# Kernel optimization log

Hardware: AMD Instinct MI355X
Metric: run time of the kernel (lower is better)

Reference implementation:

```python
import jax, jax.numpy as jnp
import numpy as np

B, L, N, D = 4, 288, 170, 128
HEADS = 8
WS = 12        # window_size
SHIFT = 6      # shift_size
HID = 4 * D    # mlp hidden
NW = L // WS   # num windows
HD = D // HEADS
SCALE = HD ** -0.5
EPS = 1e-5


def _layernorm(x, g, b):
    m = jnp.mean(x, axis=-1, keepdims=True)
    v = jnp.mean(jnp.square(x - m), axis=-1, keepdims=True)
    return (x - m) * jax.lax.rsqrt(v + EPS) * g + b


def _attn_mask():
    # labels: [0:SHIFT]->0, [SHIFT:WS]->1, [WS:]->2 along L, then windowed
    idx = jnp.arange(L)
    lab = jnp.where(idx < SHIFT, 0.0, jnp.where(idx < WS, 1.0, 2.0)).astype(jnp.float32)
    mw = lab.reshape(NW, WS)                      # (nW, ws)
    diff = mw[:, None, :] - mw[:, :, None]        # (nW, ws, ws)
    return jnp.where(diff != 0, -100.0, 0.0)


def setup_inputs() -> dict:
    key = jax.random.key(0)
    ks = jax.random.split(key, 8)
    w = 0.02
    return {
        "x": jax.random.normal(ks[0], (B, L, N, D), jnp.float32),
        "qkv_w": jax.random.normal(ks[1], (D, 3 * D), jnp.float32) * w,
        "qkv_b": jnp.zeros((3 * D,), jnp.float32),
        "proj_w": jax.random.normal(ks[2], (D, D), jnp.float32) * w,
        "proj_b": jnp.zeros((D,), jnp.float32),
        "fc1_w": jax.random.normal(ks[3], (D, HID), jnp.float32) * w,
        "fc1_b": jnp.zeros((HID,), jnp.float32),
        "fc2_w": jax.random.normal(ks[4], (HID, D), jnp.float32) * w,
        "fc2_b": jnp.zeros((D,), jnp.float32),
        "g1": jnp.ones((D,), jnp.float32),
        "b1": jnp.zeros((D,), jnp.float32),
        "g2": jnp.ones((D,), jnp.float32),
        "b2": jnp.zeros((D,), jnp.float32),
    }


def reference(x, qkv_w, qkv_b, proj_w, proj_b, fc1_w, fc1_b, fc2_w, fc2_b, g1, b1, g2, b2):
    mask = _attn_mask()                                  # (nW, ws, ws)
    x = jnp.transpose(x, (0, 2, 1, 3))                   # (B, N, L, D)
    residual = x
    # shift + window partition
    sx = jnp.roll(x, SHIFT, axis=2)
    xw = sx.reshape(B, N, NW, WS, D).transpose(0, 2, 1, 3, 4).reshape(B * NW, N, WS, D)
    # windowed MSA
    qkv = xw @ qkv_w + qkv_b                             # (B_, N, ws, 3D)
    qkv = qkv.reshape(B * NW, N, WS, 3, HEADS, HD).transpose(3, 0, 4, 1, 2, 5)
    q, k, v = qkv[0], qkv[1], qkv[2]                     # (B_, H, N, ws, hd)
    attn = jnp.einsum('bhnwd,bhnvd->bhnwv', q * SCALE, k)
    attn = attn.reshape(B, NW, HEADS, N, WS, WS) + mask[None, :, None, None]
    attn = jax.nn.softmax(attn.reshape(B * NW, HEADS, N, WS, WS), axis=-1)
    out = jnp.einsum('bhnwv,bhnvd->bhnwd', attn, v)      # (B_, H, N, ws, hd)
    out = out.transpose(0, 2, 3, 1, 4).reshape(B * NW, N, WS, D)
    out = out @ proj_w + proj_b
    # window reverse + unshift
    shifted = out.reshape(B, NW, N, WS, D).transpose(0, 2, 1, 3, 4).reshape(B, N, L, D)
    xa = jnp.roll(shifted, -SHIFT, axis=2)
    # post-norm residuals
    x = residual + _layernorm(xa, g1, b1)
    h = jax.nn.gelu(x @ fc1_w + fc1_b, approximate=False) @ fc2_w + fc2_b
    x = x + _layernorm(h, g2, b2)
    return jnp.transpose(x, (0, 2, 1, 3))                # (B, L, N, D)
```

## Files before the change

kernel.cpp:

```cpp
#include <hip/hip_runtime.h>
#include <cmath>

namespace {
constexpr int kB = 4;
constexpr int kL = 288;
constexpr int kN = 170;
constexpr int kD = 128;
constexpr int kHeads = 8;
constexpr int kWS = 12;
constexpr int kShift = 6;
constexpr int kHid = 512;
constexpr int kNW = 24;
constexpr int kHD = 16;
constexpr float kScale = 0.25f;
constexpr float kEps = 1e-5f;
constexpr int kTokens = kB * kL * kN;
constexpr int kGroups = kB * kNW * kN;
}

typedef __attribute__((ext_vector_type(8))) short bf16x8;
typedef __attribute__((ext_vector_type(4))) short bf16x4;
typedef __attribute__((ext_vector_type(4))) float f32x4;

__device__ inline short f2bf(float f) {
  union { float f; unsigned u; } v; v.f = f;
  const unsigned r = v.u + 0x7fffu + ((v.u >> 16) & 1u);
  return (short)(r >> 16);
}
__device__ inline float bf2f(short s) {
  union { unsigned u; float f; } v;
  v.u = ((unsigned)(unsigned short)s) << 16;
  return v.f;
}

__global__ __launch_bounds__(256) void prep_weights_kernel(
    const float* __restrict__ fc1_w, const float* __restrict__ fc2_w,
    const float* __restrict__ qkv_w, const float* __restrict__ proj_w,
    short* __restrict__ fc1_wt, short* __restrict__ fc2_wt,
    short* __restrict__ qkv_wt, short* __restrict__ proj_wt)
{
  const int i = blockIdx.x * 256 + threadIdx.x;
  if (i < kD * kHid) {
    { const int c = i >> 7, k = i & 127; fc1_wt[i] = f2bf(fc1_w[k * kHid + c]); }
    { const int c = i >> 9, k = i & 511; fc2_wt[i] = f2bf(fc2_w[k * kD + c]); }
  }
  if (qkv_wt != nullptr) {
    if (i < 384 * kD) { const int c = i >> 7, k = i & 127; qkv_wt[i]  = f2bf(qkv_w[k * 384 + c]); }
    if (i < kD * kD)  { const int c = i >> 7, k = i & 127; proj_wt[i] = f2bf(proj_w[k * kD + c]); }
  }
}

__global__ __launch_bounds__(256) void qkv_mfma_kernel(
    const float* __restrict__ x,
    const short* __restrict__ qkv_wt,
    const float* __restrict__ qkv_b,
    short* __restrict__ qkvb)
{
  const int t0 = blockIdx.x * 32;
  const int tid = threadIdx.x;
  const int wave = tid >> 6, lane = tid & 63;
  const int g = lane >> 4, r16 = lane & 15;

  bf16x8 bfrag[2][4];
#pragma unroll
  for (int tt = 0; tt < 2; ++tt) {
    const int row = t0 + tt * 16 + r16;
    const int grp = row / 12, j = row - grp * 12;
    const int n = grp % kN;
    const int bw = grp / kN;
    const int w = bw % kNW, b = bw / kNW;
    int l = w * kWS + j - kShift; if (l < 0) l += kL;
    const float* xp = x + (((size_t)b * kL + l) * kN + n) * kD + g * 8;
#pragma unroll
    for (int s = 0; s < 4; ++s) {
      const float4 lo = *(const float4*)(xp + 32 * s);
      const float4 hi = *(const float4*)(xp + 32 * s + 4);
      bf16x8 bb;
      bb[0] = f2bf(lo.x); bb[1] = f2bf(lo.y); bb[2] = f2bf(lo.z); bb[3] = f2bf(lo.w);
      bb[4] = f2bf(hi.x); bb[5] = f2bf(hi.y); bb[6] = f2bf(hi.z); bb[7] = f2bf(hi.w);
      bfrag[tt][s] = bb;
    }
  }

  const int c0 = wave * 96;
#pragma unroll 2
  for (int m = 0; m < 6; ++m) {
    const int cbase = c0 + m * 16;
    const short* wp = qkv_wt + (size_t)(cbase + r16) * kD + g * 8;
    const float4 bv = *(const float4*)(qkv_b + cbase + g * 4);
    f32x4 acc0 = {bv.x, bv.y, bv.z, bv.w};
    f32x4 acc1 = acc0;
#pragma unroll
    for (int s = 0; s < 4; ++s) {
      const bf16x8 a = *(const bf16x8*)(wp + 32 * s);
      acc0 = __builtin_amdgcn_mfma_f32_16x16x32_bf16(a, bfrag[0][s], acc0, 0, 0, 0);
      acc1 = __builtin_amdgcn_mfma_f32_16x16x32_bf16(a, bfrag[1][s], acc1, 0, 0, 0);
    }
#pragma unroll
    for (int tt = 0; tt < 2; ++tt) {
      const f32x4 v = tt ? acc1 : acc0;
      bf16x4 pk;
#pragma unroll
      for (int r = 0; r < 4; ++r) pk[r] = f2bf(v[r]);
      const int row = t0 + tt * 16 + r16;
      *(bf16x4*)(qkvb + (size_t)row * 384 + cbase + g * 4) = pk;
    }
  }
}

__global__ __launch_bounds__(256) void attn_core_kernel(
    const short* __restrict__ qkvb,
    const short* __restrict__ proj_wt,
    const float* __restrict__ proj_b,
    const float* __restrict__ x,
    const float* __restrict__ g1, const float* __restrict__ b1,
    float* __restrict__ x1)
{
  constexpr int NB = 4;
  constexpr int NT = NB * kWS;
  const int blk = blockIdx.x;
  const int tid = threadIdx.x;

  __shared__ __align__(16) char smem[NT * 384 * 2 + NT * kD * 2];
  short* const qs  = (short*)smem;
  char*  const aoc = smem + NT * 384 * 2;
  char*  const poc = smem;
  __shared__ float mu_s[NT], rs_s[NT];

  {
    const bf16x8* src = (const bf16x8*)(qkvb + (size_t)blk * NT * 384);
    bf16x8* dst = (bf16x8*)qs;
#pragma unroll
    for (int e = 0; e < 9; ++e) dst[e * 256 + tid] = src[e * 256 + tid];
  }
  __syncthreads();

  for (int task = tid; task < NB * 96; task += 256) {
    const int g = task / 96;
    const int rem = task - g * 96;
    const int h = rem / 12;
    const int i = rem - h * 12;
    const int gg = blk * NB + g;
    const bool edge = ((gg / kN) % kNW) == 0;
    const short* base = qs + g * 12 * 384;

    const bf16x8 q0 = *(const bf16x8*)(base + i * 384 + h * 16);
    const bf16x8 q1 = *(const bf16x8*)(base + i * 384 + h * 16 + 8);
    float q[16];
#pragma unroll
    for (int d = 0; d < 8; ++d) { q[d] = bf2f(q0[d]) * kScale; q[8 + d] = bf2f(q1[d]) * kScale; }

    float p[12];
    float m = -1e30f;
#pragma unroll
    for (int j = 0; j < 12; ++j) {
      const bf16x8 k0 = *(const bf16x8*)(base + j * 384 + 128 + h * 16);
      const bf16x8 k1 = *(const bf16x8*)(base + j * 384 + 128 + h * 16 + 8);
      float s = 0.f;
#pragma unroll
      for (int d = 0; d < 8; ++d) s += q[d] * bf2f(k0[d]) + q[8 + d] * bf2f(k1[d]);
      if (edge && ((i < 6) != (j < 6))) s -= 100.f;
      p[j] = s;
      m = fmaxf(m, s);
    }
    float sum = 0.f;
#pragma unroll
    for (int j = 0; j < 12; ++j) { p[j] = expf(p[j] - m); sum += p[j]; }
    const float inv = 1.f / sum;

    float acc[16];
#pragma unroll
    for (int d = 0; d < 16; ++d) acc[d] = 0.f;
#pragma unroll
    for (int j = 0; j < 12; ++j) {
      const bf16x8 v0 = *(const bf16x8*)(base + j * 384 + 256 + h * 16);
      const bf16x8 v1 = *(const bf16x8*)(base + j * 384 + 256 + h * 16 + 8);
      const float pj = p[j] * inv;
#pragma unroll
      for (int d = 0; d < 8; ++d) { acc[d] += pj * bf2f(v0[d]); acc[8 + d] += pj * bf2f(v1[d]); }
    }
    const int t = g * 12 + i;
    bf16x8 o0, o1;
#pragma unroll
    for (int d = 0; d < 8; ++d) { o0[d] = f2bf(acc[d]); o1[d] = f2bf(acc[8 + d]); }
    const unsigned swz = (unsigned)((t & 7) << 4);
    *(bf16x8*)(aoc + (((unsigned)(t * 256 + h * 32)) ^ swz)) = o0;
    *(bf16x8*)(aoc + (((unsigned)(t * 256 + h * 32 + 16)) ^ swz)) = o1;
  }
  __syncthreads();

  {
    const int wave = tid >> 6, lane = tid & 63;
    const int g4 = lane >> 4, r16 = lane & 15;
    const int cb0 = wave * 32;
    f32x4 acc[2][3];
#pragma unroll
    for (int mm = 0; mm < 2; ++mm) {
      const float4 bv = *(const float4*)(proj_b + cb0 + mm * 16 + g4 * 4);
      const f32x4 bi = {bv.x, bv.y, bv.z, bv.w};
      acc[mm][0] = bi; acc[mm][1] = bi; acc[mm][2] = bi;
    }
#pragma unroll
    for (int s = 0; s < 4; ++s) {
      bf16x8 afr[2], bfr[3];
#pragma unroll
      for (int mm = 0; mm < 2; ++mm)
        afr[mm] = *(const bf16x8*)(proj_wt + (size_t)(cb0 + mm * 16 + r16) * kD + s * 32 + g4 * 8);
#pragma unroll
      for (int tt = 0; tt < 3; ++tt) {
        const int t = tt * 16 + r16;
        const unsigned boff = ((unsigned)(t * 256 + s * 64 + g4 * 16)) ^ ((unsigned)((t & 7) << 4));
        bfr[tt] = *(const bf16x8*)(aoc + boff);
      }
#pragma unroll
      for (int mm = 0; mm < 2; ++mm)
#pragma unroll
        for (int tt = 0; tt < 3; ++tt)
          acc[mm][tt] = __builtin_amdgcn_mfma_f32_16x16x32_bf16(afr[mm], bfr[tt], acc[mm][tt], 0, 0, 0);
    }
#pragma unroll
    for (int mm = 0; mm < 2; ++mm)
#pragma unroll
      for (int tt = 0; tt < 3; ++tt) {
        const int t = tt * 16 + r16;
        const int c = cb0 + mm * 16 + g4 * 4;
        const unsigned poff = ((unsigned)(t * 512 + c * 4)) ^ ((unsigned)((t & 7) << 4));
        *(f32x4*)(poc + poff) = acc[mm][tt];
      }
  }
  __syncthreads();

  {
    const int tok = tid >> 2;
    const int seg = tid & 3;
    if (tok < NT) {
      const unsigned swz = (unsigned)((tok & 7) << 4);
      float s1 = 0.f, s2 = 0.f;
#pragma unroll
      for (int qd = 0; qd < 32; ++qd) {
        const int c = seg * 32 + qd;
        const float v = *(const float*)(poc + (((unsigned)(tok * 512 + c * 4)) ^ swz));
        s1 += v; s2 += v * v;
      }
#pragma unroll
      for (int d = 1; d < 4; d <<= 1) { s1 += __shfl_xor(s1, d); s2 += __shfl_xor(s2, d); }
      if (seg == 0) {
        const float mu = s1 * (1.f / kD);
        const float var = s2 * (1.f / kD) - mu * mu;
        mu_s[tok] = mu;
        rs_s[tok] = rsqrtf(var + kEps);
      }
    }
  }
  __syncthreads();

  for (int e = tid; e < NT * kD; e += 256) {
    const int t = e >> 7, c = e & 127;
    const float v = *(const float*)(poc +
        (((unsigned)(t * 512 + c * 4)) ^ ((unsigned)((t & 7) << 4))));
    const int gg = blk * NB + t / 12;
    const int j = t - (t / 12) * 12;
    const int n = gg % kN;
    const int bw = gg / kN;
    const int w = bw % kNW, b = bw / kNW;
    int l = w * kWS + j - kShift; if (l < 0) l += kL;
    const size_t idx = (((size_t)b * kL + l) * kN + n) * kD + c;
    x1[idx] = (v - mu_s[t]) * rs_s[t] * g1[c] + b1[c] + x[idx];
  }
}

__global__ __launch_bounds__(384) void swin_attn_kernel(
    const float* __restrict__ x,
    const float* __restrict__ qkv_w, const float* __restrict__ qkv_b,
    const float* __restrict__ proj_w, const float* __restrict__ proj_b,
    const float* __restrict__ g1, const float* __restrict__ b1,
    float* __restrict__ x1)
{
  const int blk = blockIdx.x;
  const int n = blk % kN;
  const int bw = blk / kN;
  const int w = bw % kNW;
  const int b = bw / kNW;
  const int tid = threadIdx.x;

  __shared__ float xsT[kD][kWS];
  __shared__ float qkv_s[kWS][3 * kD];
  __shared__ float S[kHeads][kWS][kWS];
  __shared__ float aoT[kD][kWS];
  __shared__ float po[kWS][kD];
  __shared__ float mu_s[kWS], rs_s[kWS];

  for (int e = tid; e < kWS * kD; e += 384) {
    const int j = e / kD, d = e % kD;
    const int l = (w * kWS + j - kShift + kL) % kL;
    xsT[d][j] = x[(((size_t)b * kL + l) * kN + n) * kD + d];
  }
  __syncthreads();

  {
    const int c = tid;
    float acc[kWS];
    const float bias = qkv_b[c];
#pragma unroll
    for (int j = 0; j < kWS; ++j) acc[j] = bias;
    for (int k = 0; k < kD; ++k) {
      const float wv = qkv_w[k * 384 + c];
      const float4* xr = (const float4*)&xsT[k][0];
      const float4 a0 = xr[0], a1 = xr[1], a2 = xr[2];
      acc[0] += a0.x * wv; acc[1] += a0.y * wv; acc[2]  += a0.z * wv; acc[3]  += a0.w * wv;
      acc[4] += a1.x * wv; acc[5] += a1.y * wv; acc[6]  += a1.z * wv; acc[7]  += a1.w * wv;
      acc[8] += a2.x * wv; acc[9] += a2.y * wv; acc[10] += a2.z * wv; acc[11] += a2.w * wv;
    }
#pragma unroll
    for (int j = 0; j < kWS; ++j) qkv_s[j][c] = acc[j];
  }
  __syncthreads();

  for (int e = tid; e < kHeads * kWS * kWS; e += 384) {
    const int h = e / (kWS * kWS);
    const int r = e % (kWS * kWS);
    const int i = r / kWS, j = r % kWS;
    const float* qp = &qkv_s[i][h * kHD];
    const float* kp = &qkv_s[j][kD + h * kHD];
    float s = 0.f;
#pragma unroll
    for (int d = 0; d < kHD; ++d) s += qp[d] * kp[d];
    s *= kScale;
    if (w == 0 && ((i < kShift) != (j < kShift))) s -= 100.f;
    S[h][i][j] = s;
  }
  __syncthreads();

  if (tid < kHeads * kWS) {
    const int h = tid / kWS, i = tid % kWS;
    float m = -1e30f;
#pragma unroll
    for (int j = 0; j < kWS; ++j) m = fmaxf(m, S[h][i][j]);
    float p[kWS];
    float sum = 0.f;
#pragma unroll
    for (int j = 0; j < kWS; ++j) { p[j] = expf(S[h][i][j] - m); sum += p[j]; }
    const float inv = 1.f / sum;
#pragma unroll
    for (int j = 0; j < kWS; ++j) S[h][i][j] = p[j] * inv;
  }
  __syncthreads();

  for (int e = tid; e < kWS * kD; e += 384) {
    const int i = e / kD, c = e % kD;
    const int h = c / kHD;
    float s = 0.f;
#pragma unroll
    for (int j = 0; j < kWS; ++j) s += S[h][i][j] * qkv_s[j][2 * kD + c];
    aoT[c][i] = s;
  }
  __syncthreads();

  {
    const int c = tid % kD;
    const int g = tid / kD;
    const float bias = proj_b[c];
    float acc0 = bias, acc1 = bias, acc2 = bias, acc3 = bias;
    for (int k = 0; k < kD; ++k) {
      const float wv = proj_w[k * kD + c];
      const float4 a = *(const float4*)&aoT[k][4 * g];
      acc0 += a.x * wv; acc1 += a.y * wv; acc2 += a.z * wv; acc3 += a.w * wv;
    }
    po[4 * g + 0][c] = acc0;
    po[4 * g + 1][c] = acc1;
    po[4 * g + 2][c] = acc2;
    po[4 * g + 3][c] = acc3;
  }
  __syncthreads();

  if (tid < kWS) {
    const int i = tid;
    float s = 0.f, ss = 0.f;
    for (int c = 0; c < kD; ++c) { const float v = po[i][c]; s += v; ss += v * v; }
    const float mu = s * (1.f / kD);
    const float var = ss * (1.f / kD) - mu * mu;
    mu_s[i] = mu;
    rs_s[i] = rsqrtf(var + kEps);
  }
  __syncthreads();

  for (int e = tid; e < kWS * kD; e += 384) {
    const int i = e / kD, c = e % kD;
    const int l = (w * kWS + i - kShift + kL) % kL;
    const size_t idx = (((size_t)b * kL + l) * kN + n) * kD + c;
    x1[idx] = (po[i][c] - mu_s[i]) * rs_s[i] * g1[c] + b1[c] + x[idx];
  }
}

__global__ __launch_bounds__(256) void mlp_mfma_kernel(
    const float* __restrict__ x1,
    const short* __restrict__ fc1_wt,
    const short* __restrict__ fc2_wt,
    const float* __restrict__ fc1_b, const float* __restrict__ fc2_b,
    const float* __restrict__ g2, const float* __restrict__ b2,
    float* __restrict__ out)
{
  constexpr int TM = 32;
  const int t0 = blockIdx.x * TM;
  const int tid = threadIdx.x;
  const int wave = tid >> 6;
  const int lane = tid & 63;
  const int g = lane >> 4;
  const int r16 = lane & 15;

  __shared__ short hs[TM * kHid];
  __shared__ float po[TM][kD];
  __shared__ float mu_s[TM], rs_s[TM];
  char* const hbase = (char*)hs;

  bf16x8 bfrag[2][4];
#pragma unroll
  for (int tt = 0; tt < 2; ++tt) {
    const float* xp = x1 + (size_t)(t0 + tt * 16 + r16) * kD + g * 8;
#pragma unroll
    for (int s = 0; s < 4; ++s) {
      const float4 lo = *(const float4*)(xp + 32 * s);
      const float4 hi = *(const float4*)(xp + 32 * s + 4);
      bf16x8 bb;
      bb[0] = f2bf(lo.x); bb[1] = f2bf(lo.y); bb[2] = f2bf(lo.z); bb[3] = f2bf(lo.w);
      bb[4] = f2bf(hi.x); bb[5] = f2bf(hi.y); bb[6] = f2bf(hi.z); bb[7] = f2bf(hi.w);
      bfrag[tt][s] = bb;
    }
  }

  const int c0 = wave * 128;
#pragma unroll 2
  for (int m = 0; m < 8; ++m) {
    const int cbase = c0 + m * 16;
    const short* wp = fc1_wt + (size_t)(cbase + r16) * kD + g * 8;
    const float4 bias = *(const float4*)(fc1_b + cbase + g * 4);
    f32x4 acc0 = {bias.x, bias.y, bias.z, bias.w};
    f32x4 acc1 = acc0;
#pragma unroll
    for (int s = 0; s < 4; ++s) {
      const bf16x8 a = *(const bf16x8*)(wp + 32 * s);
      acc0 = __builtin_amdgcn_mfma_f32_16x16x32_bf16(a, bfrag[0][s], acc0, 0, 0, 0);
      acc1 = __builtin_amdgcn_mfma_f32_16x16x32_bf16(a, bfrag[1][s], acc1, 0, 0, 0);
    }
#pragma unroll
    for (int tt = 0; tt < 2; ++tt) {
      const f32x4 v = tt ? acc1 : acc0;
      bf16x4 p;
#pragma unroll
      for (int r = 0; r < 4; ++r) {
        const float z = v[r];
        p[r] = f2bf(0.5f * z * (1.f + erff(z * 0.70710678118654752f)));
      }
      const int t_local = tt * 16 + r16;
      unsigned off = (unsigned)((t_local * kHid + cbase + g * 4) * 2);
      off ^= (unsigned)((t_local & 7) << 4);
      *(bf16x4*)(hbase + off) = p;
    }
  }
  __syncthreads();

  const int n0 = wave * 32;
  f32x4 acc[2][2];
#pragma unroll
  for (int nt = 0; nt < 2; ++nt) {
    const float bv = fc2_b[n0 + nt * 16 + r16];
    acc[0][nt] = {bv, bv, bv, bv};
    acc[1][nt] = acc[0][nt];
  }
#pragma unroll 4
  for (int s = 0; s < 16; ++s) {
    bf16x8 afr[2];
#pragma unroll
    for (int tt = 0; tt < 2; ++tt) {
      const int t_local = tt * 16 + r16;
      unsigned off = (unsigned)((t_local * kHid + s * 32 + g * 8) * 2);
      off ^= (unsigned)((t_local & 7) << 4);
      afr[tt] = *(const bf16x8*)(hbase + off);
    }
#pragma unroll
    for (int nt = 0; nt < 2; ++nt) {
      const bf16x8 bfr = *(const bf16x8*)(fc2_wt + (size_t)(n0 + nt * 16 + r16) * kHid + s * 32 + g * 8);
      acc[0][nt] = __builtin_amdgcn_mfma_f32_16x16x32_bf16(afr[0], bfr, acc[0][nt], 0, 0, 0);
      acc[1][nt] = __builtin_amdgcn_mfma_f32_16x16x32_bf16(afr[1], bfr, acc[1][nt], 0, 0, 0);
    }
  }
#pragma unroll
  for (int tt = 0; tt < 2; ++tt)
#pragma unroll
    for (int nt = 0; nt < 2; ++nt)
#pragma unroll
      for (int r = 0; r < 4; ++r)
        po[tt * 16 + g * 4 + r][n0 + nt * 16 + r16] = acc[tt][nt][r];
  __syncthreads();

  {
    const int tok = tid >> 3;
    const int seg = tid & 7;
    float s1 = 0.f, s2 = 0.f;
    const float* pr = &po[tok][seg * 16];
#pragma unroll
    for (int q = 0; q < 16; ++q) { const float v = pr[q]; s1 += v; s2 += v * v; }
#pragma unroll
    for (int d = 1; d < 8; d <<= 1) {
      s1 += __shfl_xor(s1, d);
      s2 += __shfl_xor(s2, d);
    }
    if (seg == 0) {
      const float mu = s1 * (1.f / kD);
      const float var = s2 * (1.f / kD) - mu * mu;
      mu_s[tok] = mu;
      rs_s[tok] = rsqrtf(var + kEps);
    }
  }
  __syncthreads();

  {
    const int tok = tid >> 3;
    const int cb = (tid & 7) * 16;
    const float mu = mu_s[tok], rs = rs_s[tok];
    const size_t gbase = (size_t)(t0 + tok) * kD + cb;
#pragma unroll
    for (int q = 0; q < 16; ++q) {
      const int c = cb + q;
      out[gbase + q] = (po[tok][c] - mu) * rs * g2[c] + b2[c] + x1[gbase + q];
    }
  }
}

extern "C" void kernel_launch(void* const* d_in, const int* in_sizes, int n_in,
                              void* d_out, int out_size, void* d_ws, size_t ws_size,
                              hipStream_t stream) {
  const float* x      = (const float*)d_in[0];
  const float* qkv_w  = (const float*)d_in[1];
  const float* qkv_b  = (const float*)d_in[2];
  const float* proj_w = (const float*)d_in[3];
  const float* proj_b = (const float*)d_in[4];
  const float* fc1_w  = (const float*)d_in[5];
  const float* fc1_b  = (const float*)d_in[6];
  const float* fc2_w  = (const float*)d_in[7];
  const float* fc2_b  = (const float*)d_in[8];
  const float* g1     = (const float*)d_in[9];
  const float* b1     = (const float*)d_in[10];
  const float* g2     = (const float*)d_in[11];
  const float* b2     = (const float*)d_in[12];
  float* out = (float*)d_out;

  float* x1 = (float*)d_ws;
  const size_t need_new = (size_t)kTokens * kD * 4
                        + (size_t)kTokens * 384 * 2
                        + (size_t)(384 * kD + kD * kD + kHid * kD + kD * kHid) * 2;

  if (ws_size >= need_new) {
    short* qkvb    = (short*)(x1 + (size_t)kTokens * kD);
    short* qkv_wt  = qkvb + (size_t)kTokens * 384;
    short* proj_wt = qkv_wt + 384 * kD;
    short* fc1_wt  = proj_wt + kD * kD;
    short* fc2_wt  = fc1_wt + kHid * kD;

    prep_weights_kernel<<<256, 256, 0, stream>>>(fc1_w, fc2_w, qkv_w, proj_w,
                                                 fc1_wt, fc2_wt, qkv_wt, proj_wt);
    qkv_mfma_kernel<<<kTokens / 32, 256, 0, stream>>>(x, qkv_wt, qkv_b, qkvb);
    attn_core_kernel<<<kGroups / 4, 256, 0, stream>>>(qkvb, proj_wt, proj_b, x,
                                                      g1, b1, x1);
    mlp_mfma_kernel<<<kTokens / 32, 256, 0, stream>>>(x1, fc1_wt, fc2_wt, fc1_b,
                                                      fc2_b, g2, b2, out);
  } else {
    short* fc1_wt = (short*)(x1 + (size_t)kTokens * kD);
    short* fc2_wt = fc1_wt + kD * kHid;
    prep_weights_kernel<<<256, 256, 0, stream>>>(fc1_w, fc2_w, nullptr, nullptr,
                                                 fc1_wt, fc2_wt, nullptr, nullptr);
    swin_attn_kernel<<<kGroups, 384, 0, stream>>>(x, qkv_w, qkv_b, proj_w, proj_b,
                                                  g1, b1, x1);
    mlp_mfma_kernel<<<kTokens / 32, 256, 0, stream>>>(x1, fc1_wt, fc2_wt, fc1_b,
                                                      fc2_b, g2, b2, out);
  }
}
```

Baseline: 681.6 us.

## Use packed bf16 conversion, fast tanh GELU, padded LDS strides, vectorized epilogue

Replaces scalar float-to-bf16 rounding with paired hardware conversions. Swaps the erf-based GELU for a tanh-form approximation built on exp2 and rcp. Pads the shared-memory strides for the qkv tile and the fp32 projection/MLP outputs to reduce bank conflicts, replacing the XOR swizzle. Vectorizes the final residual load and output store with float4. The GELU approximation changes numerics slightly relative to the exact erf version.

```diff
diff --git a/kernel.cpp b/kernel.cpp
--- a/kernel.cpp
+++ b/kernel.cpp
@@ -1,4 +1,5 @@
 #include <hip/hip_runtime.h>
+#include <hip/hip_bf16.h>
 #include <cmath>
 
 namespace {
@@ -16,6 +17,8 @@
 constexpr float kEps = 1e-5f;
 constexpr int kTokens = kB * kL * kN;
 constexpr int kGroups = kB * kNW * kN;
+constexpr int kQSStr = 400;
+constexpr int kPOStr = 129;
 }
 
 typedef __attribute__((ext_vector_type(8))) short bf16x8;
@@ -27,10 +30,22 @@
   const unsigned r = v.u + 0x7fffu + ((v.u >> 16) & 1u);
   return (short)(r >> 16);
 }
+__device__ inline unsigned f2bf2(float lo, float hi) {
+  union { __hip_bfloat162 h; unsigned u; } cv;
+  cv.h = __float22bfloat162_rn(make_float2(lo, hi));
+  return cv.u;
+}
 __device__ inline float bf2f(short s) {
   union { unsigned u; float f; } v;
   v.u = ((unsigned)(unsigned short)s) << 16;
   return v.f;
+}
+__device__ inline float gelu_fast(float z) {
+  const float z2 = z * z;
+  const float u  = z * fmaf(0.044715f, z2, 1.0f);
+  const float t  = exp2f(2.3022082f * u);
+  const float r  = __builtin_amdgcn_rcpf(t + 1.0f);
+  return fmaf(-z, r, z);
 }
 
 __global__ __launch_bounds__(256) void prep_weights_kernel(
@@ -75,10 +90,10 @@
     for (int s = 0; s < 4; ++s) {
       const float4 lo = *(const float4*)(xp + 32 * s);
       const float4 hi = *(const float4*)(xp + 32 * s + 4);
-      bf16x8 bb;
-      bb[0] = f2bf(lo.x); bb[1] = f2bf(lo.y); bb[2] = f2bf(lo.z); bb[3] = f2bf(lo.w);
-      bb[4] = f2bf(hi.x); bb[5] = f2bf(hi.y); bb[6] = f2bf(hi.z); bb[7] = f2bf(hi.w);
-      bfrag[tt][s] = bb;
+      union { bf16x8 v; unsigned u[4]; } bb;
+      bb.u[0] = f2bf2(lo.x, lo.y); bb.u[1] = f2bf2(lo.z, lo.w);
+      bb.u[2] = f2bf2(hi.x, hi.y); bb.u[3] = f2bf2(hi.z, hi.w);
+      bfrag[tt][s] = bb.v;
     }
   }
 
@@ -99,11 +114,10 @@
 #pragma unroll
     for (int tt = 0; tt < 2; ++tt) {
       const f32x4 v = tt ? acc1 : acc0;
-      bf16x4 pk;
-#pragma unroll
-      for (int r = 0; r < 4; ++r) pk[r] = f2bf(v[r]);
+      union { bf16x4 v4; unsigned u[2]; } pk;
+      pk.u[0] = f2bf2(v[0], v[1]); pk.u[1] = f2bf2(v[2], v[3]);
       const int row = t0 + tt * 16 + r16;
-      *(bf16x4*)(qkvb + (size_t)row * 384 + cbase + g * 4) = pk;
+      *(bf16x4*)(qkvb + (size_t)row * 384 + cbase + g * 4) = pk.v4;
     }
   }
 }
@@ -121,17 +135,20 @@
   const int blk = blockIdx.x;
   const int tid = threadIdx.x;
 
-  __shared__ __align__(16) char smem[NT * 384 * 2 + NT * kD * 2];
+  __shared__ __align__(16) char smem[NT * kQSStr * 2 + NT * kD * 2];
   short* const qs  = (short*)smem;
-  char*  const aoc = smem + NT * 384 * 2;
-  char*  const poc = smem;
+  char*  const aoc = smem + NT * kQSStr * 2;
+  float* const pof = (float*)smem;
   __shared__ float mu_s[NT], rs_s[NT];
 
   {
-    const bf16x8* src = (const bf16x8*)(qkvb + (size_t)blk * NT * 384);
-    bf16x8* dst = (bf16x8*)qs;
-#pragma unroll
-    for (int e = 0; e < 9; ++e) dst[e * 256 + tid] = src[e * 256 + tid];
+    const short* src = qkvb + (size_t)blk * NT * 384;
+#pragma unroll
+    for (int e0 = 0; e0 < 9; ++e0) {
+      const int e = e0 * 256 + tid;
+      const int row = e / 48, u = e - row * 48;
+      *(bf16x8*)(qs + row * kQSStr + u * 8) = *(const bf16x8*)(src + e * 8);
+    }
   }
   __syncthreads();
 
@@ -142,10 +159,10 @@
     const int i = rem - h * 12;
     const int gg = blk * NB + g;
     const bool edge = ((gg / kN) % kNW) == 0;
-    const short* base = qs + g * 12 * 384;
-
-    const bf16x8 q0 = *(const bf16x8*)(base + i * 384 + h * 16);
-    const bf16x8 q1 = *(const bf16x8*)(base + i * 384 + h * 16 + 8);
+    const short* base = qs + g * 12 * kQSStr;
+
+    const bf16x8 q0 = *(const bf16x8*)(base + i * kQSStr + h * 16);
+    const bf16x8 q1 = *(const bf16x8*)(base + i * kQSStr + h * 16 + 8);
     float q[16];
 #pragma unroll
     for (int d = 0; d < 8; ++d) { q[d] = bf2f(q0[d]) * kScale; q[8 + d] = bf2f(q1[d]) * kScale; }
@@ -154,8 +171,8 @@
     float m = -1e30f;
 #pragma unroll
     for (int j = 0; j < 12; ++j) {
-      const bf16x8 k0 = *(const bf16x8*)(base + j * 384 + 128 + h * 16);
-      const bf16x8 k1 = *(const bf16x8*)(base + j * 384 + 128 + h * 16 + 8);
+      const bf16x8 k0 = *(const bf16x8*)(base + j * kQSStr + 128 + h * 16);
+      const bf16x8 k1 = *(const bf16x8*)(base + j * kQSStr + 128 + h * 16 + 8);
       float s = 0.f;
 #pragma unroll
       for (int d = 0; d < 8; ++d) s += q[d] * bf2f(k0[d]) + q[8 + d] * bf2f(k1[d]);
@@ -173,19 +190,22 @@
     for (int d = 0; d < 16; ++d) acc[d] = 0.f;
 #pragma unroll
     for (int j = 0; j < 12; ++j) {
-      const bf16x8 v0 = *(const bf16x8*)(base + j * 384 + 256 + h * 16);
-      const bf16x8 v1 = *(const bf16x8*)(base + j * 384 + 256 + h * 16 + 8);
+      const bf16x8 v0 = *(const bf16x8*)(base + j * kQSStr + 256 + h * 16);
+      const bf16x8 v1 = *(const bf16x8*)(base + j * kQSStr + 256 + h * 16 + 8);
       const float pj = p[j] * inv;
 #pragma unroll
       for (int d = 0; d < 8; ++d) { acc[d] += pj * bf2f(v0[d]); acc[8 + d] += pj * bf2f(v1[d]); }
     }
     const int t = g * 12 + i;
-    bf16x8 o0, o1;
-#pragma unroll
-    for (int d = 0; d < 8; ++d) { o0[d] = f2bf(acc[d]); o1[d] = f2bf(acc[8 + d]); }
+    union { bf16x8 v; unsigned u[4]; } o0, o1;
+#pragma unroll
+    for (int d = 0; d < 4; ++d) {
+      o0.u[d] = f2bf2(acc[2 * d], acc[2 * d + 1]);
+      o1.u[d] = f2bf2(acc[8 + 2 * d], acc[9 + 2 * d]);
+    }
     const unsigned swz = (unsigned)((t & 7) << 4);
-    *(bf16x8*)(aoc + (((unsigned)(t * 256 + h * 32)) ^ swz)) = o0;
-    *(bf16x8*)(aoc + (((unsigned)(t * 256 + h * 32 + 16)) ^ swz)) = o1;
+    *(bf16x8*)(aoc + (((unsigned)(t * 256 + h * 32)) ^ swz)) = o0.v;
+    *(bf16x8*)(aoc + (((unsigned)(t * 256 + h * 32 + 16)) ^ swz)) = o1.v;
   }
   __syncthreads();
 
@@ -224,8 +244,9 @@
       for (int tt = 0; tt < 3; ++tt) {
         const int t = tt * 16 + r16;
         const int c = cb0 + mm * 16 + g4 * 4;
-        const unsigned poff = ((unsigned)(t * 512 + c * 4)) ^ ((unsigned)((t & 7) << 4));
-        *(f32x4*)(poc + poff) = acc[mm][tt];
+#pragma unroll
+        for (int r = 0; r < 4; ++r)
+          pof[t * kPOStr + c + r] = acc[mm][tt][r];
       }
   }
   __syncthreads();
@@ -234,14 +255,10 @@
     const int tok = tid >> 2;
     const int seg = tid & 3;
     if (tok < NT) {
-      const unsigned swz = (unsigned)((tok & 7) << 4);
       float s1 = 0.f, s2 = 0.f;
-#pragma unroll
-      for (int qd = 0; qd < 32; ++qd) {
-        const int c = seg * 32 + qd;
-        const float v = *(const float*)(poc + (((unsigned)(tok * 512 + c * 4)) ^ swz));
-        s1 += v; s2 += v * v;
-      }
+      const float* pr = pof + tok * kPOStr + seg * 32;
+#pragma unroll
+      for (int qd = 0; qd < 32; ++qd) { const float v = pr[qd]; s1 += v; s2 += v * v; }
 #pragma unroll
       for (int d = 1; d < 4; d <<= 1) { s1 += __shfl_xor(s1, d); s2 += __shfl_xor(s2, d); }
       if (seg == 0) {
@@ -256,10 +273,10 @@
 
   for (int e = tid; e < NT * kD; e += 256) {
     const int t = e >> 7, c = e & 127;
-    const float v = *(const float*)(poc +
-        (((unsigned)(t * 512 + c * 4)) ^ ((unsigned)((t & 7) << 4))));
-    const int gg = blk * NB + t / 12;
-    const int j = t - (t / 12) * 12;
+    const float v = pof[t * kPOStr + c];
+    const int gl = t / 12;
+    const int j = t - gl * 12;
+    const int gg = blk * NB + gl;
     const int n = gg % kN;
     const int bw = gg / kN;
     const int w = bw % kNW, b = bw / kNW;
@@ -409,7 +426,7 @@
   const int r16 = lane & 15;
 
   __shared__ short hs[TM * kHid];
-  __shared__ float po[TM][kD];
+  __shared__ float po[TM][kD + 1];
   __shared__ float mu_s[TM], rs_s[TM];
   char* const hbase = (char*)hs;
 
@@ -421,10 +438,10 @@
     for (int s = 0; s < 4; ++s) {
       const float4 lo = *(const float4*)(xp + 32 * s);
       const float4 hi = *(const float4*)(xp + 32 * s + 4);
-      bf16x8 bb;
-      bb[0] = f2bf(lo.x); bb[1] = f2bf(lo.y); bb[2] = f2bf(lo.z); bb[3] = f2bf(lo.w);
-      bb[4] = f2bf(hi.x); bb[5] = f2bf(hi.y); bb[6] = f2bf(hi.z); bb[7] = f2bf(hi.w);
-      bfrag[tt][s] = bb;
+      union { bf16x8 v; unsigned u[4]; } bb;
+      bb.u[0] = f2bf2(lo.x, lo.y); bb.u[1] = f2bf2(lo.z, lo.w);
+      bb.u[2] = f2bf2(hi.x, hi.y); bb.u[3] = f2bf2(hi.z, hi.w);
+      bfrag[tt][s] = bb.v;
     }
   }
 
@@ -445,16 +462,13 @@
 #pragma unroll
     for (int tt = 0; tt < 2; ++tt) {
       const f32x4 v = tt ? acc1 : acc0;
-      bf16x4 p;
-#pragma unroll
-      for (int r = 0; r < 4; ++r) {
-        const float z = v[r];
-        p[r] = f2bf(0.5f * z * (1.f + erff(z * 0.70710678118654752f)));
-      }
+      union { bf16x4 v4; unsigned u[2]; } p;
+      p.u[0] = f2bf2(gelu_fast(v[0]), gelu_fast(v[1]));
+      p.u[1] = f2bf2(gelu_fast(v[2]), gelu_fast(v[3]));
       const int t_local = tt * 16 + r16;
       unsigned off = (unsigned)((t_local * kHid + cbase + g * 4) * 2);
       off ^= (unsigned)((t_local & 7) << 4);
-      *(bf16x4*)(hbase + off) = p;
+      *(bf16x4*)(hbase + off) = p.v4;
     }
   }
   __syncthreads();
@@ -520,9 +534,15 @@
     const float mu = mu_s[tok], rs = rs_s[tok];
     const size_t gbase = (size_t)(t0 + tok) * kD + cb;
 #pragma unroll
-    for (int q = 0; q < 16; ++q) {
-      const int c = cb + q;
-      out[gbase + q] = (po[tok][c] - mu) * rs * g2[c] + b2[c] + x1[gbase + q];
+    for (int q4 = 0; q4 < 4; ++q4) {
+      const int c = cb + 4 * q4;
+      const float4 rx = *(const float4*)(x1 + gbase + 4 * q4);
+      float4 o;
+      o.x = (po[tok][c + 0] - mu) * rs * g2[c + 0] + b2[c + 0] + rx.x;
+      o.y = (po[tok][c + 1] - mu) * rs * g2[c + 1] + b2[c + 1] + rx.y;
+      o.z = (po[tok][c + 2] - mu) * rs * g2[c + 2] + b2[c + 2] + rx.z;
+      o.w = (po[tok][c + 3] - mu) * rs * g2[c + 3] + b2[c + 3] + rx.w;
+      *(float4*)(out + gbase + 4 * q4) = o;
     }
   }
 }
```

Result: no change. 683.8 us (+0.3%).
